# Optimization experiments

Measured on AMD Instinct MI355X. Metric: run time of the kernel, lower is better.

## Reference

```python
import jax, jax.numpy as jnp
import numpy as np

R = 4          # corr_radius
SLOPE = 0.1    # leaky relu negative slope


def _conv(x, w, b, pad):
    y = jax.lax.conv_general_dilated(
        x, w, window_strides=(1, 1), padding=[(pad, pad), (pad, pad)],
        dimension_numbers=("NCHW", "OIHW", "NCHW"))
    return y + b[None, :, None, None]


def _correlation(x1, x2):
    # Fused windowed cost volume: cv[b, i*(2R+1)+j, h, w] = mean_c x1[b,c,h,w] * x2[b,c,h+i-R,w+j-R]
    B, C, H, W = x1.shape
    x2p = jnp.pad(x2, ((0, 0), (0, 0), (R, R), (R, R)))
    cv = jnp.stack(
        [jnp.mean(x1 * jax.lax.dynamic_slice(x2p, (0, 0, i, j), (B, C, H, W)), axis=1)
         for i in range(2 * R + 1) for j in range(2 * R + 1)], axis=1)
    return cv  # (B, (2R+1)^2, H, W)


def setup_inputs() -> dict:
    key = jax.random.key(0)
    ks = jax.random.split(key, 20)
    B, H, W = 2, 256, 256
    pyr = 24
    inp = {
        "feat0": jax.random.normal(ks[0], (B, 2 * pyr, H, W), jnp.float32),
        "feat1": jax.random.normal(ks[1], (B, 2 * pyr, H, W), jnp.float32),
        "last_feat": jax.random.normal(ks[2], (B, 64, H, W), jnp.float32),
        "last_flow": jax.random.normal(ks[3], (B, 4, H, W), jnp.float32),
    }
    in_ch = (2 * R + 1) ** 2 + 2 * (2 * pyr) + 64 + 4  # 245
    dims = [(160, in_ch, 1), (128, 160, 3), (112, 128, 3), (96, 112, 3), (64, 96, 3), (4, 64, 3)]
    for n, (co, ci, k) in enumerate(dims, 1):
        scale = 1.0 / np.sqrt(ci * k * k)
        inp[f"w{n}"] = jax.random.normal(ks[4 + 2 * n], (co, ci, k, k), jnp.float32) * scale
        inp[f"b{n}"] = jnp.zeros((co,), jnp.float32)
    return inp


def reference(feat0, feat1, last_feat, last_flow,
              w1, b1, w2, b2, w3, b3, w4, b4, w5, b5, w6, b6):
    lrelu = lambda x: jax.nn.leaky_relu(x, SLOPE)
    volume = lrelu(_correlation(feat0, feat1))
    feat = jnp.concatenate([volume, feat0, feat1, last_feat, last_flow], axis=1)
    x = lrelu(_conv(feat, w1, b1, 0))   # 1x1 conv
    x = lrelu(_conv(x, w2, b2, 1))
    x = lrelu(_conv(x, w3, b3, 1))
    x = lrelu(_conv(x, w4, b4, 1))
    x = lrelu(_conv(x, w5, b5, 1))
    flow = _conv(x, w6, b6, 1)          # final ConvBlock, act=None
    return flow, x
```

## Files before the change

kernel.cpp:

```cpp
#include <hip/hip_runtime.h>
#include <hip/hip_fp16.h>
#include <cstdint>
#include <cstddef>


using short8 = __attribute__((ext_vector_type(8))) short;
using f32x4  = __attribute__((ext_vector_type(4))) float;
typedef unsigned short u16;

__device__ __forceinline__ u16 rne_bf16(float f) {
  unsigned u = __float_as_uint(f);
  u += 0x7FFFu + ((u >> 16) & 1u);
  return (u16)(u >> 16);
}

__device__ __forceinline__ void mfma16(const short8& a, const short8& b, f32x4& c) {
  asm("v_mfma_f32_16x16x32_bf16 %0, %1, %2, %0" : "+v"(c) : "v"(a), "v"(b));
}

__device__ __forceinline__ unsigned pk_f16(float a, float b) {
  unsigned r;
  asm("v_cvt_pkrtz_f16_f32 %0, %1, %2" : "=v"(r) : "v"(a), "v"(b));
  return r;
}

__device__ __forceinline__ void dot2(float& acc, unsigned a, unsigned b) {
  asm("v_dot2_f32_f16 %0, %1, %2, %0" : "+v"(acc) : "v"(a), "v"(b));
}

__device__ __forceinline__ void gload16(const void* g, void* l) {
  __builtin_amdgcn_global_load_lds(
      (const __attribute__((address_space(1))) unsigned int*)g,
      (__attribute__((address_space(3))) unsigned int*)l, 16, 0, 0);
}

__device__ __forceinline__ uint2 quad_to_bf16(uint2 v) {
  __half2 lo = *(__half2*)&v.x, hi = *(__half2*)&v.y;
  uint2 u;
  u.x = (unsigned)rne_bf16(__half2float(lo.x)) | ((unsigned)rne_bf16(__half2float(lo.y)) << 16);
  u.y = (unsigned)rne_bf16(__half2float(hi.x)) | ((unsigned)rne_bf16(__half2float(hi.y)) << 16);
  return u;
}

__global__ __launch_bounds__(256) void prep1_kernel(const float* __restrict__ w1,
                                                    u16* __restrict__ w1p) {
  int idx = blockIdx.x * 256 + threadIdx.x;
  int co = idx >> 8, cip = idx & 255;
  float v = 0.f;
  if (co < 160 && cip < 245) {
    int ci = (cip < 164) ? (cip + 81) : (cip - 164);
    v = w1[co * 245 + ci];
  }
  w1p[idx] = rne_bf16(v);
}

template<int CO, int CIr, int BM, int APLN, int CIP>
__global__ __launch_bounds__(256) void prep3s_kernel(const float* __restrict__ w,
                                                     u16* __restrict__ wp) {
  int idx = blockIdx.x * 256 + threadIdx.x;
  int ci = idx % CIP; int rest = idx / CIP;
  int row = rest % APLN; int dyp = rest / APLN;
  int dx = row / BM, co = row % BM;
  float v = 0.f;
  if (dx < 3 && co < CO && ci < CIr)
    v = w[(co * CIr + ci) * 9 + dyp * 3 + dx];
  wp[idx] = rne_bf16(v);
}

__global__ __launch_bounds__(256) void prep_bias_kernel(const float* __restrict__ b1,
    const float* __restrict__ b2, const float* __restrict__ b3,
    const float* __restrict__ b4, const float* __restrict__ b5,
    const float* __restrict__ b6,
    float* __restrict__ bp, u16* __restrict__ zbuf) {
  int i = blockIdx.x * 256 + threadIdx.x;
  if (i < 128) zbuf[i] = 0;
  float v = 0.f;
  if (i < 160) v = b1[i];
  else if (i < 288) v = b2[i - 160];
  else if (i < 416) { int c = i - 288; v = (c < 112) ? b3[c] : 0.f; }
  else if (i < 512) v = b4[i - 416];
  else if (i < 576) v = b5[i - 512];
  else if (i < 608) { int c = i - 576; v = (c < 4) ? b6[c] : 0.f; }
  else return;
  bp[i] = v;
}

__global__ __launch_bounds__(256) void quadize_kernel(const float* __restrict__ f0,
                                                      const float* __restrict__ f1,
                                                      u16* __restrict__ f0q,
                                                      u16* __restrict__ f1q) {
  const int bid = blockIdx.x;
  const int qh = bid >> 9;
  const int b = (bid >> 8) & 1;
  const int h = bid & 255;
  const int hw = (h << 8) + threadIdx.x;
  const float* s0 = f0 + (((size_t)(b * 48 + qh * 24)) << 16) + hw;
  const float* s1 = f1 + (((size_t)(b * 48 + qh * 24)) << 16) + hw;
  u16* d0 = f0q + (((size_t)((b * 12 + qh * 6) << 16)) + hw) * 4;
  u16* d1 = f1q + (((size_t)((b * 12 + qh * 6) << 16)) + hw) * 4;
#pragma unroll
  for (int q = 0; q < 6; ++q) {
    uint2 u;
    u.x = pk_f16(s0[((size_t)(4 * q)) << 16],     s0[((size_t)(4 * q + 1)) << 16]);
    u.y = pk_f16(s0[((size_t)(4 * q + 2)) << 16], s0[((size_t)(4 * q + 3)) << 16]);
    *(uint2*)(d0 + (size_t)q * 262144) = u;
    uint2 v;
    v.x = pk_f16(s1[((size_t)(4 * q)) << 16],     s1[((size_t)(4 * q + 1)) << 16]);
    v.y = pk_f16(s1[((size_t)(4 * q + 2)) << 16], s1[((size_t)(4 * q + 3)) << 16]);
    *(uint2*)(d1 + (size_t)q * 262144) = v;
  }
}

__global__ __launch_bounds__(256) void concat68_kernel(const float* __restrict__ lf,
                                                       const float* __restrict__ lfl,
                                                       u16* __restrict__ X1) {
  __shared__ float s[16][68];
  const int t = threadIdx.x;
  const size_t px0 = (size_t)blockIdx.x * 64;
  const int b = blockIdx.x >> 10;
  const int hw0 = (blockIdx.x & 1023) * 64;

#pragma unroll 1
  for (int cc = 0; cc < 5; ++cc) {
    __syncthreads();
    {
      int px = t & 63, cg = t >> 6;
#pragma unroll
      for (int r = 0; r < 4; ++r) {
        int cl = cg * 4 + r;
        int c = cc * 16 + cl;
        int hw = hw0 + px;
        float v = 0.f;
        if (c < 64)       v = lf[(((size_t)(b * 64 + c)) << 16) + hw];
        else if (c < 68)  v = lfl[(((size_t)(b * 4 + (c - 64))) << 16) + hw];
        s[cl][px] = v;
      }
    }
    __syncthreads();
    {
      int px = t >> 2, g = t & 3;
      int cbase = cc * 16 + g * 4;
      if (cbase < 68) {
        ushort4 u;
        u.x = rne_bf16(s[g * 4 + 0][px]);
        u.y = rne_bf16(s[g * 4 + 1][px]);
        u.z = rne_bf16(s[g * 4 + 2][px]);
        u.w = rne_bf16(s[g * 4 + 3][px]);
        *(ushort4*)(X1 + (px0 + px) * 256 + 96 + cbase) = u;
      }
    }
  }
}

template<int NDY>
__device__ __forceinline__ void corr_acc(const uint2* __restrict__ wb,
                                         const unsigned* __restrict__ f0p,
                                         float* __restrict__ cv,
                                         int row, int col, int dy0) {
#pragma unroll
  for (int d = 0; d < NDY; ++d) {
    const int r = row + dy0 + d;
#pragma unroll
    for (int q = 0; q < 3; ++q) {
      const uint2* base = wb + (q * 10 + r) * 80 + (col + 4);
#pragma unroll
      for (int dx = 0; dx < 9; ++dx) {
        const uint2 v = base[dx];
        dot2(cv[d * 9 + dx], v.x, f0p[2 * q]);
        dot2(cv[d * 9 + dx], v.y, f0p[2 * q + 1]);
      }
    }
  }
}

__global__ __launch_bounds__(256, 4) void corr5_kernel(const u16* __restrict__ f0q,
                                                       const u16* __restrict__ f1q,
                                                       const u16* __restrict__ zbuf,
                                                       u16* __restrict__ X1) {
  __shared__ char wlds[2][20480];
  const int bid = blockIdx.x;
  const int swz = (bid & 7) * 128 + (bid >> 3);
  const int b = swz >> 9, rest = swz & 511;
  const int hp = rest >> 2, ct = rest & 3;
  const int h0 = hp << 1, w0 = ct << 6;
  const int tid = threadIdx.x, lane = tid & 63, wv = tid >> 6;
  const int half = wv >> 1, row = wv & 1, col = lane;
  const int pixhw = ((h0 + row) << 8) + (w0 + col);
  const size_t pix = ((size_t)b << 16) + pixhw;

  const u16* srcp[5];
  bool okf[5];
#pragma unroll
  for (int ru = 0; ru < 5; ++ru) {
    int u = ru * 256 + tid;
    int uq = u / 400;
    int rem = u - uq * 400;
    int r = rem / 40, cu = rem - r * 40;
    int hin = h0 + r - 4;
    int wpx = w0 - 8 + 2 * cu;
    bool ok = (u < 1200) && ((unsigned)hin < 256u) && ((unsigned)wpx < 256u);
    okf[ru] = ok;
    srcp[ru] = ok ? (f1q + (((size_t)((b * 12 + uq) << 16) + (hin << 8) + wpx) << 2))
                  : zbuf;
  }

  float cv[45];
#pragma unroll
  for (int t = 0; t < 45; ++t) cv[t] = 0.f;

#pragma unroll
  for (int ru = 0; ru < 5; ++ru)
    gload16(srcp[ru], &wlds[0][ru * 4096 + wv * 1024]);

#pragma unroll 1
  for (int cc = 0; cc < 4; ++cc) {
    __syncthreads();
    if (cc < 3) {
#pragma unroll
      for (int ru = 0; ru < 5; ++ru) {
        const u16* s = okf[ru] ? (srcp[ru] + (size_t)(cc + 1) * 786432) : zbuf;
        gload16(s, &wlds[(cc + 1) & 1][ru * 4096 + wv * 1024]);
      }
    }
    const uint2* wb = (const uint2*)&wlds[cc & 1][0];

    const u16* f0base = f0q + (((size_t)((b * 12 + cc * 3) << 16) + pixhw) << 2);
    uint2 q0 = *(const uint2*)(f0base);
    uint2 q1 = *(const uint2*)(f0base + 262144);
    uint2 q2 = *(const uint2*)(f0base + 524288);
    unsigned f0p[6] = {q0.x, q0.y, q1.x, q1.y, q2.x, q2.y};

    {
      u16* dst0 = X1 + pix * 256 + cc * 12;
      *(uint2*)(dst0)     = quad_to_bf16(q0);
      *(uint2*)(dst0 + 4) = quad_to_bf16(q1);
      *(uint2*)(dst0 + 8) = quad_to_bf16(q2);
    }
    {
      u16* dst1 = X1 + pix * 256 + 48 + cc * 12;
#pragma unroll
      for (int q = 0; q < 3; ++q) {
        uint2 v = wb[(q * 10 + row + 4) * 80 + (col + 8)];
        *(uint2*)(dst1 + 4 * q) = quad_to_bf16(v);
      }
    }
    if (half == 0) corr_acc<4>(wb, f0p, cv, row, col, 0);
    else           corr_acc<5>(wb, f0p, cv, row, col, 4);
  }

  u16* dst = X1 + pix * 256;
  const float sc = 1.0f / 48.0f;
  if (half == 0) {
#pragma unroll
    for (int qq = 0; qq < 9; ++qq) {
      u16 e[4];
#pragma unroll
      for (int j = 0; j < 4; ++j) {
        float v = cv[qq * 4 + j] * sc;
        v = v > 0.f ? v : 0.1f * v;
        e[j] = rne_bf16(v);
      }
      uint2 u;
      u.x = (unsigned)e[0] | ((unsigned)e[1] << 16);
      u.y = (unsigned)e[2] | ((unsigned)e[3] << 16);
      *(uint2*)(dst + 164 + qq * 4) = u;
    }
  } else {
#pragma unroll
    for (int qq = 0; qq < 14; ++qq) {
      u16 e[4];
#pragma unroll
      for (int j = 0; j < 4; ++j) {
        int t = qq * 4 + j;
        float v = 0.f;
        if (t < 45) {
          v = cv[t] * sc;
          v = v > 0.f ? v : 0.1f * v;
        }
        e[j] = rne_bf16(v);
      }
      uint2 u;
      u.x = (unsigned)e[0] | ((unsigned)e[1] << 16);
      u.y = (unsigned)e[2] | ((unsigned)e[3] << 16);
      *(uint2*)(dst + 200 + qq * 4) = u;
    }
  }
}

template<int CI, int BM, int APLN, int KS, int OSTRIDE, bool LRELU, bool OBF, int COF32>
__global__ __launch_bounds__(256, 2) void convr_kernel(const u16* __restrict__ Xin,
    const u16* __restrict__ Wp, const float* __restrict__ bias,
    const u16* __restrict__ zbuf, u16* __restrict__ Xout,
    float* __restrict__ outF) {
  constexpr int NCH = CI / 32;
  constexpr int NDX = (KS == 3) ? 3 : 1;
  constexpr int HALO = (KS == 3) ? 2 : 0;
  constexpr int AROUNDS = APLN / 64;
  constexpr int BROUNDS = (KS == 3) ? 5 : 4;
  constexpr int BPXMAX = 256 + 2 * HALO;
  constexpr int MF = BM / 32;
  constexpr int AELEMS = AROUNDS * 2048;
  constexpr int NPH = NDX * NCH;
  __shared__ u16 lds[AELEMS + BROUNDS * 2048];

  const int tid = threadIdx.x;
  const int lane = tid & 63, wv = tid >> 6;
  const int wm = wv >> 1, wn = wv & 1;
  const int bid = blockIdx.x;
  const int swz = (bid & 7) * 64 + (bid >> 3);
  const int bi = swz >> 8;
  const int h = swz & 255;
  const int l15 = lane & 15, segr = lane >> 4;

  size_t aofs[AROUNDS];
#pragma unroll
  for (int r = 0; r < AROUNDS; ++r) {
    int slot = r * 256 + tid;
    int row = slot >> 2, sp = slot & 3;
    int seg = sp ^ ((row >> 1) & 3);
    aofs[r] = (size_t)row * CI + seg * 8;
  }
  size_t bofs[BROUNDS];
  bool bcolv[BROUNDS];
#pragma unroll
  for (int r = 0; r < BROUNDS; ++r) {
    int slot = r * 256 + tid;
    int pxl = slot >> 2, sp = slot & 3;
    int seg = sp ^ ((pxl >> 1) & 3);
    int px = pxl - HALO;
    bcolv[r] = ((unsigned)px < 256u) && (pxl < BPXMAX);
    bofs[r] = (size_t)px * CI + seg * 8;
  }

  f32x4 acc[MF][8];
  const f32x4 zf = {0.f, 0.f, 0.f, 0.f};
#pragma unroll
  for (int m = 0; m < MF; ++m)
#pragma unroll
    for (int n = 0; n < 8; ++n) acc[m][n] = zf;

  int dy = 0, c = 0;
#pragma unroll 1
  for (int ph = 0; ph < NPH; ++ph) {
    __syncthreads();
    const u16* Wph = Wp + ((size_t)dy * APLN) * CI + c * 32;
#pragma unroll
    for (int r = 0; r < AROUNDS; ++r)
      gload16(Wph + aofs[r], &lds[r * 2048 + wv * 512]);
    const int hin = (KS == 3) ? (h + dy - 1) : h;
    const bool rv = (unsigned)hin < 256u;
    const u16* Brow = Xin + ((size_t)((bi << 8) + (rv ? hin : 0)) << 8) * CI + c * 32;
#pragma unroll
    for (int r = 0; r < BROUNDS; ++r) {
      const u16* src = (rv && bcolv[r]) ? (Brow + bofs[r]) : zbuf;
      gload16(src, &lds[AELEMS + r * 2048 + wv * 512]);
    }
    __syncthreads();

#pragma unroll
    for (int dx = 0; dx < NDX; ++dx) {
      short8 bfr[8];
#pragma unroll
      for (int n = 0; n < 8; ++n) {
        int p = wn * 128 + n * 16 + l15;
        int pxl = (KS == 3) ? (p + dx + 1) : p;
        int ba = (AELEMS * 2) + pxl * 64 + ((segr ^ ((pxl >> 1) & 3)) << 4);
        bfr[n] = *(const short8*)((const char*)lds + ba);
      }
      short8 afr[MF];
#pragma unroll
      for (int m = 0; m < MF; ++m) {
        int row = dx * BM + wm * (BM / 2) + m * 16 + l15;
        int aa = row * 64 + ((segr ^ ((row >> 1) & 3)) << 4);
        afr[m] = *(const short8*)((const char*)lds + aa);
      }
#pragma unroll
      for (int m = 0; m < MF; ++m)
#pragma unroll
        for (int n = 0; n < 8; ++n) mfma16(afr[m], bfr[n], acc[m][n]);
    }
    if (++c == NCH) { c = 0; ++dy; }
  }
  asm volatile("s_nop 7\n\ts_nop 7");

  const int co_sub = (lane >> 4) << 2;
  const size_t pixbase = ((size_t)((bi << 8) + h)) << 8;
#pragma unroll
  for (int m = 0; m < MF; ++m) {
    const int co = wm * (BM / 2) + m * 16 + co_sub;
#pragma unroll
    for (int n = 0; n < 8; ++n) {
      const int px = wn * 128 + n * 16 + l15;
      f32x4 v = acc[m][n];
      float t[4];
#pragma unroll
      for (int r = 0; r < 4; ++r) {
        float x = v[r] + bias[co + r];
        if (LRELU) x = x > 0.f ? x : 0.1f * x;
        t[r] = x;
      }
      if (OBF) {
        ushort4 u;
        u.x = rne_bf16(t[0]); u.y = rne_bf16(t[1]);
        u.z = rne_bf16(t[2]); u.w = rne_bf16(t[3]);
        *(ushort4*)(Xout + (pixbase + px) * OSTRIDE + co) = u;
      }
      if (COF32 > 0) {
#pragma unroll
        for (int r = 0; r < 4; ++r) {
          int cch = co + r;
          if (cch < COF32)
            outF[(((size_t)bi * COF32 + cch) << 16) + (h << 8) + px] = t[r];
        }
      }
    }
  }
}

extern "C" void kernel_launch(void* const* d_in, const int* in_sizes, int n_in,
                              void* d_out, int out_size, void* d_ws, size_t ws_size,
                              hipStream_t stream) {
  const float* feat0 = (const float*)d_in[0];
  const float* feat1 = (const float*)d_in[1];
  const float* lfeat = (const float*)d_in[2];
  const float* lflow = (const float*)d_in[3];
  const float* w1 = (const float*)d_in[4];  const float* b1 = (const float*)d_in[5];
  const float* w2 = (const float*)d_in[6];  const float* b2 = (const float*)d_in[7];
  const float* w3 = (const float*)d_in[8];  const float* b3 = (const float*)d_in[9];
  const float* w4 = (const float*)d_in[10]; const float* b4 = (const float*)d_in[11];
  const float* w5 = (const float*)d_in[12]; const float* b5 = (const float*)d_in[13];
  const float* w6 = (const float*)d_in[14]; const float* b6 = (const float*)d_in[15];

  u16* ws = (u16*)d_ws;
  u16* X1 = ws;
  u16* X2 = ws + 33554432;
  u16* X3 = ws;
  u16* X4 = ws + 33554432;
  u16* X5 = ws;
  u16* X6 = ws + 33554432;
  u16* f0q = ws + 33554432;
  u16* f1q = ws + 39845888;
  u16* w1p = ws + 54525952;
  u16* w2p = w1p + 49152;
  u16* w3p = w2p + 184320;
  u16* w4p = w3p + 147456;
  u16* w5p = w4p + 147456;
  u16* w6p = w5p + 55296;
  float* bp = (float*)(w6p + 24576);
  u16* zbuf = (u16*)(bp + 608);

  const float* bp1 = bp;
  const float* bp2 = bp + 160;
  const float* bp3 = bp + 288;
  const float* bp4 = bp + 416;
  const float* bp5 = bp + 512;
  const float* bp6 = bp + 576;

  float* flow = (float*)d_out;
  float* xout = (float*)d_out + 524288;

  prep1_kernel<<<192, 256, 0, stream>>>(w1, w1p);
  prep3s_kernel<128, 160, 128, 384, 160><<<720, 256, 0, stream>>>(w2, w2p);
  prep3s_kernel<112, 128, 128, 384, 128><<<576, 256, 0, stream>>>(w3, w3p);
  prep3s_kernel< 96, 112,  96, 320, 128><<<480, 256, 0, stream>>>(w4, w4p);
  prep3s_kernel< 64,  96,  64, 192,  96><<<216, 256, 0, stream>>>(w5, w5p);
  prep3s_kernel<  4,  64,  32, 128,  64><<< 96, 256, 0, stream>>>(w6, w6p);
  prep_bias_kernel<<<3, 256, 0, stream>>>(b1, b2, b3, b4, b5, b6, bp, zbuf);

  quadize_kernel<<<1024, 256, 0, stream>>>(feat0, feat1, f0q, f1q);
  concat68_kernel<<<2048, 256, 0, stream>>>(lfeat, lflow, X1);
  corr5_kernel<<<1024, 256, 0, stream>>>(f0q, f1q, zbuf, X1);

  convr_kernel<256, 160, 192, 1, 160, true,  true,  0><<<512, 256, 0, stream>>>(X1, w1p, bp1, zbuf, X2, nullptr);
  convr_kernel<160, 128, 384, 3, 128, true,  true,  0><<<512, 256, 0, stream>>>(X2, w2p, bp2, zbuf, X3, nullptr);
  convr_kernel<128, 128, 384, 3, 128, true,  true,  0><<<512, 256, 0, stream>>>(X3, w3p, bp3, zbuf, X4, nullptr);
  convr_kernel<128,  96, 320, 3,  96, true,  true,  0><<<512, 256, 0, stream>>>(X4, w4p, bp4, zbuf, X5, nullptr);
  convr_kernel< 96,  64, 192, 3,  64, true,  true, 64><<<512, 256, 0, stream>>>(X5, w5p, bp5, zbuf, X6, xout);
  convr_kernel< 64,  32, 128, 3,   1, false, false, 4><<<512, 256, 0, stream>>>(X6, w6p, bp6, zbuf, nullptr, flow);
}
```

Measured before the change: 282.5 us.

## Switch conv kernels to 32x32x16 bf16 MFMA with per-wave pixel split

Replaces the 16x16x32 MFMA tiling with 32x32x16 MFMA in all six conv layers. Each wave now covers all output channels and a 64-pixel slice, instead of the previous 2x2 split over channels and pixels. The goal is to cut LDS fragment reads per flop and raise MFMA throughput per instruction. In exchange, every wave now re-reads the full weight tile, which duplicates weight-fragment traffic. The last layer (BM=32, 4 real channels) also does more padded work per wave.

```diff
diff --git a/kernel.cpp b/kernel.cpp
--- a/kernel.cpp
+++ b/kernel.cpp
@@ -6,6 +6,7 @@
 
 using short8 = __attribute__((ext_vector_type(8))) short;
 using f32x4  = __attribute__((ext_vector_type(4))) float;
+using f32x16 = __attribute__((ext_vector_type(16))) float;
 typedef unsigned short u16;
 
 __device__ __forceinline__ u16 rne_bf16(float f) {
@@ -14,8 +15,8 @@
   return (u16)(u >> 16);
 }
 
-__device__ __forceinline__ void mfma16(const short8& a, const short8& b, f32x4& c) {
-  asm("v_mfma_f32_16x16x32_bf16 %0, %1, %2, %0" : "+v"(c) : "v"(a), "v"(b));
+__device__ __forceinline__ void mfma32(const short8& a, const short8& b, f32x16& c) {
+  asm("v_mfma_f32_32x32x16_bf16 %0, %1, %2, %0" : "+v"(c) : "v"(a), "v"(b));
 }
 
 __device__ __forceinline__ unsigned pk_f16(float a, float b) {
@@ -288,7 +289,7 @@
 }
 
 template<int CI, int BM, int APLN, int KS, int OSTRIDE, bool LRELU, bool OBF, int COF32>
-__global__ __launch_bounds__(256, 2) void convr_kernel(const u16* __restrict__ Xin,
+__global__ __launch_bounds__(256, 2) void convr32_kernel(const u16* __restrict__ Xin,
     const u16* __restrict__ Wp, const float* __restrict__ bias,
     const u16* __restrict__ zbuf, u16* __restrict__ Xout,
     float* __restrict__ outF) {
@@ -298,19 +299,18 @@
   constexpr int AROUNDS = APLN / 64;
   constexpr int BROUNDS = (KS == 3) ? 5 : 4;
   constexpr int BPXMAX = 256 + 2 * HALO;
-  constexpr int MF = BM / 32;
+  constexpr int MF32 = BM / 32;
   constexpr int AELEMS = AROUNDS * 2048;
   constexpr int NPH = NDX * NCH;
   __shared__ u16 lds[AELEMS + BROUNDS * 2048];
 
   const int tid = threadIdx.x;
-  const int lane = tid & 63, wv = tid >> 6;
-  const int wm = wv >> 1, wn = wv & 1;
+  const int lane = tid & 63, wn = tid >> 6;
   const int bid = blockIdx.x;
   const int swz = (bid & 7) * 64 + (bid >> 3);
   const int bi = swz >> 8;
   const int h = swz & 255;
-  const int l15 = lane & 15, segr = lane >> 4;
+  const int l31 = lane & 31, kg = lane >> 5;
 
   size_t aofs[AROUNDS];
 #pragma unroll
@@ -332,12 +332,13 @@
     bofs[r] = (size_t)px * CI + seg * 8;
   }
 
-  f32x4 acc[MF][8];
-  const f32x4 zf = {0.f, 0.f, 0.f, 0.f};
-#pragma unroll
-  for (int m = 0; m < MF; ++m)
-#pragma unroll
-    for (int n = 0; n < 8; ++n) acc[m][n] = zf;
+  f32x16 acc[MF32][2];
+#pragma unroll
+  for (int m = 0; m < MF32; ++m)
+#pragma unroll
+    for (int n = 0; n < 2; ++n)
+#pragma unroll
+      for (int e = 0; e < 16; ++e) acc[m][n][e] = 0.f;
 
   int dy = 0, c = 0;
 #pragma unroll 1
@@ -346,71 +347,77 @@
     const u16* Wph = Wp + ((size_t)dy * APLN) * CI + c * 32;
 #pragma unroll
     for (int r = 0; r < AROUNDS; ++r)
-      gload16(Wph + aofs[r], &lds[r * 2048 + wv * 512]);
+      gload16(Wph + aofs[r], &lds[r * 2048 + wn * 512]);
     const int hin = (KS == 3) ? (h + dy - 1) : h;
     const bool rv = (unsigned)hin < 256u;
     const u16* Brow = Xin + ((size_t)((bi << 8) + (rv ? hin : 0)) << 8) * CI + c * 32;
 #pragma unroll
     for (int r = 0; r < BROUNDS; ++r) {
       const u16* src = (rv && bcolv[r]) ? (Brow + bofs[r]) : zbuf;
-      gload16(src, &lds[AELEMS + r * 2048 + wv * 512]);
+      gload16(src, &lds[AELEMS + r * 2048 + wn * 512]);
     }
     __syncthreads();
 
 #pragma unroll
     for (int dx = 0; dx < NDX; ++dx) {
-      short8 bfr[8];
-#pragma unroll
-      for (int n = 0; n < 8; ++n) {
-        int p = wn * 128 + n * 16 + l15;
-        int pxl = (KS == 3) ? (p + dx + 1) : p;
-        int ba = (AELEMS * 2) + pxl * 64 + ((segr ^ ((pxl >> 1) & 3)) << 4);
-        bfr[n] = *(const short8*)((const char*)lds + ba);
-      }
-      short8 afr[MF];
-#pragma unroll
-      for (int m = 0; m < MF; ++m) {
-        int row = dx * BM + wm * (BM / 2) + m * 16 + l15;
-        int aa = row * 64 + ((segr ^ ((row >> 1) & 3)) << 4);
-        afr[m] = *(const short8*)((const char*)lds + aa);
-      }
-#pragma unroll
-      for (int m = 0; m < MF; ++m)
-#pragma unroll
-        for (int n = 0; n < 8; ++n) mfma16(afr[m], bfr[n], acc[m][n]);
+#pragma unroll
+      for (int kh = 0; kh < 2; ++kh) {
+        const int segk = kh * 2 + kg;
+        short8 bfr[2];
+#pragma unroll
+        for (int n = 0; n < 2; ++n) {
+          int p = wn * 64 + n * 32 + l31;
+          int pxl = (KS == 3) ? (p + dx + 1) : p;
+          int ba = (AELEMS * 2) + pxl * 64 + ((segk ^ ((pxl >> 1) & 3)) << 4);
+          bfr[n] = *(const short8*)((const char*)lds + ba);
+        }
+        short8 afr[MF32];
+#pragma unroll
+        for (int m = 0; m < MF32; ++m) {
+          int row = dx * BM + m * 32 + l31;
+          int aa = row * 64 + ((segk ^ ((row >> 1) & 3)) << 4);
+          afr[m] = *(const short8*)((const char*)lds + aa);
+        }
+#pragma unroll
+        for (int m = 0; m < MF32; ++m)
+#pragma unroll
+          for (int n = 0; n < 2; ++n) mfma32(afr[m], bfr[n], acc[m][n]);
+      }
     }
     if (++c == NCH) { c = 0; ++dy; }
   }
   asm volatile("s_nop 7\n\ts_nop 7");
 
-  const int co_sub = (lane >> 4) << 2;
   const size_t pixbase = ((size_t)((bi << 8) + h)) << 8;
 #pragma unroll
-  for (int m = 0; m < MF; ++m) {
-    const int co = wm * (BM / 2) + m * 16 + co_sub;
-#pragma unroll
-    for (int n = 0; n < 8; ++n) {
-      const int px = wn * 128 + n * 16 + l15;
-      f32x4 v = acc[m][n];
-      float t[4];
-#pragma unroll
-      for (int r = 0; r < 4; ++r) {
-        float x = v[r] + bias[co + r];
-        if (LRELU) x = x > 0.f ? x : 0.1f * x;
-        t[r] = x;
-      }
-      if (OBF) {
-        ushort4 u;
-        u.x = rne_bf16(t[0]); u.y = rne_bf16(t[1]);
-        u.z = rne_bf16(t[2]); u.w = rne_bf16(t[3]);
-        *(ushort4*)(Xout + (pixbase + px) * OSTRIDE + co) = u;
-      }
-      if (COF32 > 0) {
+  for (int m = 0; m < MF32; ++m) {
+#pragma unroll
+    for (int n = 0; n < 2; ++n) {
+      const int px = wn * 64 + n * 32 + l31;
+      f32x16 v = acc[m][n];
+#pragma unroll
+      for (int q = 0; q < 4; ++q) {
+        const int co = m * 32 + q * 8 + kg * 4;
+        float t[4];
 #pragma unroll
         for (int r = 0; r < 4; ++r) {
-          int cch = co + r;
-          if (cch < COF32)
-            outF[(((size_t)bi * COF32 + cch) << 16) + (h << 8) + px] = t[r];
+          float x = v[q * 4 + r] + bias[co + r];
+          if (LRELU) x = x > 0.f ? x : 0.1f * x;
+          t[r] = x;
+        }
+        if (OBF) {
+          ushort4 u;
+          u.x = rne_bf16(t[0]); u.y = rne_bf16(t[1]);
+          u.z = rne_bf16(t[2]); u.w = rne_bf16(t[3]);
+          *(ushort4*)(Xout + (pixbase + px) * OSTRIDE + co) = u;
+        }
+        if (COF32 > 0) {
+#pragma unroll
+          for (int r = 0; r < 4; ++r) {
+            int cch = co + r;
+            if (cch < COF32)
+              outF[(((size_t)bi * COF32 + cch) << 16) + (h << 8) + px] = t[r];
+          }
         }
       }
     }
@@ -471,10 +478,10 @@
   concat68_kernel<<<2048, 256, 0, stream>>>(lfeat, lflow, X1);
   corr5_kernel<<<1024, 256, 0, stream>>>(f0q, f1q, zbuf, X1);
 
-  convr_kernel<256, 160, 192, 1, 160, true,  true,  0><<<512, 256, 0, stream>>>(X1, w1p, bp1, zbuf, X2, nullptr);
-  convr_kernel<160, 128, 384, 3, 128, true,  true,  0><<<512, 256, 0, stream>>>(X2, w2p, bp2, zbuf, X3, nullptr);
-  convr_kernel<128, 128, 384, 3, 128, true,  true,  0><<<512, 256, 0, stream>>>(X3, w3p, bp3, zbuf, X4, nullptr);
-  convr_kernel<128,  96, 320, 3,  96, true,  true,  0><<<512, 256, 0, stream>>>(X4, w4p, bp4, zbuf, X5, nullptr);
-  convr_kernel< 96,  64, 192, 3,  64, true,  true, 64><<<512, 256, 0, stream>>>(X5, w5p, bp5, zbuf, X6, xout);
-  convr_kernel< 64,  32, 128, 3,   1, false, false, 4><<<512, 256, 0, stream>>>(X6, w6p, bp6, zbuf, nullptr, flow);
-}
+  convr32_kernel<256, 160, 192, 1, 160, true,  true,  0><<<512, 256, 0, stream>>>(X1, w1p, bp1, zbuf, X2, nullptr);
+  convr32_kernel<160, 128, 384, 3, 128, true,  true,  0><<<512, 256, 0, stream>>>(X2, w2p, bp2, zbuf, X3, nullptr);
+  convr32_kernel<128, 128, 384, 3, 128, true,  true,  0><<<512, 256, 0, stream>>>(X3, w3p, bp3, zbuf, X4, nullptr);
+  convr32_kernel<128,  96, 320, 3,  96, true,  true,  0><<<512, 256, 0, stream>>>(X4, w4p, bp4, zbuf, X5, nullptr);
+  convr32_kernel< 96,  64, 192, 3,  64, true,  true, 64><<<512, 256, 0, stream>>>(X5, w5p, bp5, zbuf, X6, xout);
+  convr32_kernel< 64,  32, 128, 3,   1, false, false, 4><<<512, 256, 0, stream>>>(X6, w6p, bp6, zbuf, nullptr, flow);
+}
```

Measured after the change: 294.5 us. 1.04x slower.
